# Performance work log

Hardware: AMD Instinct MI355X
Metric: run time of the kernel (lower is better)

Reference implementation:

```python
import jax, jax.numpy as jnp
import numpy as np


def lstm_step(x_t, h, c, Wih, Whh, bih, bhh):
    # PyTorch LSTM gate order: i, f, g, o
    gates = x_t @ Wih.T + h @ Whh.T + bih + bhh
    i, f, g, o = jnp.split(gates, 4, axis=-1)
    i = jax.nn.sigmoid(i)
    f = jax.nn.sigmoid(f)
    g = jnp.tanh(g)
    o = jax.nn.sigmoid(o)
    c_new = f * c + i * g
    h_new = o * jnp.tanh(c_new)
    return h_new, c_new


def setup_inputs() -> dict:
    key = jax.random.key(0)
    N, C, T, V, M = 512, 3, 300, 25, 2
    F = C * V * M  # 150
    H = 100
    ks = jax.random.split(key, 12)
    s = 1.0 / np.sqrt(H)  # PyTorch LSTM/Linear init scale
    u = lambda k, shape: jax.random.uniform(k, shape, jnp.float32, -s, s)
    return {
        "x": jax.random.normal(ks[0], (N, C, T, V, M), jnp.float32),
        "enc_Wih": u(ks[1], (4 * H, F)),
        "enc_Whh": u(ks[2], (4 * H, H)),
        "enc_bih": u(ks[3], (4 * H,)),
        "enc_bhh": u(ks[4], (4 * H,)),
        "dec_Wih": u(ks[5], (4 * H, F)),
        "dec_Whh": u(ks[6], (4 * H, H)),
        "dec_bih": u(ks[7], (4 * H,)),
        "dec_bhh": u(ks[8], (4 * H,)),
        "fc_W": u(ks[9], (F, H)),
        "fc_b": u(ks[10], (F,)),
    }


def reference(x, enc_Wih, enc_Whh, enc_bih, enc_bhh,
              dec_Wih, dec_Whh, dec_bih, dec_bhh, fc_W, fc_b):
    N, C, T, V, M = x.shape
    F = C * V * M
    H = enc_Whh.shape[1]
    # (N,C,T,V,M) -> (N,T,C*V*M)
    xs = jnp.transpose(x, (0, 2, 1, 3, 4)).reshape(N, T, F)

    # Encoder LSTM: only need final (h, c)
    h0 = jnp.zeros((N, H), x.dtype)
    c0 = jnp.zeros((N, H), x.dtype)

    def enc_step(carry, xt):
        h, c = carry
        h, c = lstm_step(xt, h, c, enc_Wih, enc_Whh, enc_bih, enc_bhh)
        return (h, c), None

    (h, c), _ = jax.lax.scan(enc_step, (h0, c0), jnp.swapaxes(xs, 0, 1))

    inp0 = jnp.zeros((N, F), x.dtype)

    def dec_step(carry, _):
        inp, h, c = carry
        h, c = lstm_step(inp, h, c, dec_Wih, dec_Whh, dec_bih, dec_bhh)
        out = h @ fc_W.T + fc_b
        return (out, h, c), out

    _, outs = jax.lax.scan(dec_step, (inp0, h, c), None, length=T - 1)  # [T-1,N,F]

    # outputs[:,0,:] stays zero, like the torch.zeros buffer
    outputs = jnp.concatenate([jnp.zeros((1, N, F), x.dtype), outs], axis=0)  # [T,N,F]
    outputs = jnp.swapaxes(outputs, 0, 1).reshape(N, T, C, V, M)
    return jnp.transpose(outputs, (0, 2, 1, 3, 4))  # (N,C,T,V,M)
```

## Files before the change

### kernel.cpp

```cpp
#include <hip/hip_runtime.h>
#include <hip/hip_fp16.h>


#define B_HIST   0u
#define HIST_STRIDE 29952
#define B_W2S    30670848u
#define B_BEFFS  30830848u
#define B_AWIH   30832448u
#define B_AENC   30975808u
#define B_ADEC1  31090496u
#define B_ADEC2  31205184u
#define B_BENCF  31319872u
#define B_B1F    31348544u
#define B_BEFFF  31377216u
#define B_XG     31405888u
#define XG_PER_BG 4300800u

typedef _Float16 f16x8 __attribute__((ext_vector_type(8)));
typedef float    f32x4 __attribute__((ext_vector_type(4)));

typedef _Float16 h2_t __attribute__((ext_vector_type(2)));
#if defined(__has_builtin)
#if __has_builtin(__builtin_amdgcn_fdot2)
#define HAS_FDOT2 1
#endif
#endif

__device__ __forceinline__ float fdot2u(unsigned a, unsigned b, float c) {
#ifdef HAS_FDOT2
  return __builtin_amdgcn_fdot2(__builtin_bit_cast(h2_t, a), __builtin_bit_cast(h2_t, b), c, false);
#else
  float al = __half2float(__ushort_as_half((unsigned short)(a & 0xffffu)));
  float ah = __half2float(__ushort_as_half((unsigned short)(a >> 16)));
  float bl = __half2float(__ushort_as_half((unsigned short)(b & 0xffffu)));
  float bh = __half2float(__ushort_as_half((unsigned short)(b >> 16)));
  return fmaf(ah, bh, fmaf(al, bl, c));
#endif
}

__device__ __forceinline__ unsigned pkrtz(float a, float b) {
  return __builtin_bit_cast(unsigned, __builtin_amdgcn_cvt_pkrtz(a, b));
}
__device__ __forceinline__ unsigned pack2f(float a, float b) {
  return (unsigned)__half_as_ushort(__float2half(a)) |
         ((unsigned)__half_as_ushort(__float2half(b)) << 16);
}
__device__ __forceinline__ float fast_sig(float x) {
  float e = __builtin_amdgcn_exp2f(x * -1.442695040888963f);
  return __builtin_amdgcn_rcpf(1.f + e);
}
__device__ __forceinline__ float fast_tanh(float x) {
  float e = __builtin_amdgcn_exp2f(x * -2.885390081777926f);
  return fmaf(2.f, __builtin_amdgcn_rcpf(1.f + e), -1.f);
}
__device__ __forceinline__ f32x4 mfma16(uint4 a, uint4 b, f32x4 c) {
  return __builtin_amdgcn_mfma_f32_16x16x32_f16(
      __builtin_bit_cast(f16x8, a), __builtin_bit_cast(f16x8, b), c, 0, 0, 0);
}
__device__ __forceinline__ float uslo(unsigned u) {
  return __half2float(__ushort_as_half((unsigned short)(u & 0xffffu)));
}
__device__ __forceinline__ float ushi(unsigned u) {
  return __half2float(__ushort_as_half((unsigned short)(u >> 16)));
}

__global__ void prep_w2(const float* __restrict__ dWih, const float* __restrict__ dWhh,
                        const float* __restrict__ dbih, const float* __restrict__ dbhh,
                        const float* __restrict__ fcW,  const float* __restrict__ fcb,
                        char* __restrict__ wsb)
{
  int idx = blockIdx.x * 256 + threadIdx.x;
  if (idx < 40000) {
    int r = idx / 100, j = idx - r * 100;
    float s = 0.f;
    for (int f = 0; f < 150; ++f) s = fmaf(dWih[r * 150 + f], fcW[f * 100 + j], s);
    ((float*)(wsb + B_W2S))[idx] = dWhh[r * 100 + j] + s;
  } else if (idx < 40400) {
    int r = idx - 40000;
    float s = 0.f;
    for (int f = 0; f < 150; ++f) s = fmaf(dWih[r * 150 + f], fcb[f], s);
    ((float*)(wsb + B_BEFFS))[r] = dbih[r] + dbhh[r] + s;
  }
}

__global__ void prep_frags(const float* __restrict__ eWih, const float* __restrict__ eWhh,
                           const float* __restrict__ dWhh,
                           const float* __restrict__ ebih, const float* __restrict__ ebhh,
                           const float* __restrict__ dbih, const float* __restrict__ dbhh,
                           char* __restrict__ wsb)
{
  int idx = blockIdx.x * 256 + threadIdx.x;
  const float* w2s = (const float*)(wsb + B_W2S);
  const float* beffs = (const float*)(wsb + B_BEFFS);
  if (idx < 8960) {
    int l = idx & 63, fi = idx >> 6;
    int kc = fi % 5, mt = fi / 5;
    int w = mt >> 2, ty = mt & 3;
    int gr = w * 16 + (l & 15);
    int r = ty * 100 + gr;
    int k0 = kc * 32 + (l >> 4) * 8;
    unsigned u[4];
    for (int p = 0; p < 4; ++p) {
      int k = k0 + 2 * p;
      float v0 = (gr < 100 && k     < 150) ? eWih[r * 150 + k]     : 0.f;
      float v1 = (gr < 100 && k + 1 < 150) ? eWih[r * 150 + k + 1] : 0.f;
      u[p] = pack2f(v0, v1);
    }
    ((uint4*)(wsb + B_AWIH))[idx] = make_uint4(u[0], u[1], u[2], u[3]);
  } else if (idx < 8960 + 3 * 7168) {
    int t = idx - 8960;
    int set = t / 7168, q = t - set * 7168;
    int l = q & 63, fi = q >> 6;
    int kc = fi & 3, mt = fi >> 2;
    int w = mt >> 2, ty = mt & 3;
    int gr = w * 16 + (l & 15);
    int r = ty * 100 + gr;
    int k0 = kc * 32 + (l >> 4) * 8;
    unsigned u[4];
    for (int p = 0; p < 4; ++p) {
      int k = k0 + 2 * p;
      float v0 = 0.f, v1 = 0.f;
      if (gr < 100) {
        if (k < 100)     v0 = set == 0 ? eWhh[r*100+k]   : set == 1 ? dWhh[r*100+k]   : w2s[r*100+k];
        if (k + 1 < 100) v1 = set == 0 ? eWhh[r*100+k+1] : set == 1 ? dWhh[r*100+k+1] : w2s[r*100+k+1];
      }
      u[p] = pack2f(v0, v1);
    }
    ((uint4*)(wsb + B_AENC + (unsigned)set * 114688u))[q] = make_uint4(u[0], u[1], u[2], u[3]);
  } else if (idx < 8960 + 21504 + 3 * 1792) {
    int t = idx - 8960 - 21504;
    int set = t / 1792, q = t - set * 1792;
    int l = q & 63, mt = q >> 6;
    int w = mt >> 2, ty = mt & 3;
    float v[4];
    for (int rr = 0; rr < 4; ++rr) {
      int gr = w * 16 + (l >> 4) * 4 + rr;
      int r = ty * 100 + gr;
      v[rr] = 0.f;
      if (gr < 100)
        v[rr] = set == 0 ? ebih[r] + ebhh[r] : set == 1 ? dbih[r] + dbhh[r] : beffs[r];
    }
    ((float4*)(wsb + B_BENCF + (unsigned)set * 28672u))[q] = make_float4(v[0], v[1], v[2], v[3]);
  }
}

__global__ __launch_bounds__(64)
void pre(const float* __restrict__ x, char* __restrict__ wsb, int nbase)
{
  const int l = threadIdx.x;
  const int tg = blockIdx.x;
  const int b  = blockIdx.y;
  const int quad = l >> 4, nn = l & 15;
  __shared__ unsigned short xls[4][16][168];

  const int t0 = tg * 4;
  const int n0 = nbase + b * 16;
  for (int it = 0; it < 84; ++it) {
    int i = l + it * 64;
    int tp = i / 1344; int rem = i - tp * 1344;
    int np = rem / 84; int p = rem - np * 84;
    unsigned val = 0;
    if (p < 75) {
      int f0 = 2 * p; int c = f0 / 50; int q = f0 - c * 50;
      const float2 v = *(const float2*)(x + (size_t)(n0 + np) * 45000 + c * 15000 + (t0 + tp) * 50 + q);
      val = pkrtz(v.x, v.y);
    }
    *(unsigned*)&xls[tp][np][2 * p] = val;
  }
  __syncthreads();

  uint4 B[4][5];
#pragma unroll
  for (int u = 0; u < 4; ++u)
#pragma unroll
    for (int kc = 0; kc < 5; ++kc)
      B[u][kc] = *(const uint4*)&xls[u][nn][kc * 32 + quad * 8];

  const uint4* awih = (const uint4*)(wsb + B_AWIH);
  const float4* bencf = (const float4*)(wsb + B_BENCF);
  unsigned short* xgo = (unsigned short*)(wsb + B_XG);

  for (int mt = 0; mt < 28; ++mt) {
    const int w = mt >> 2, ty = mt & 3;
    uint4 A0 = awih[(mt * 5 + 0) * 64 + l];
    uint4 A1 = awih[(mt * 5 + 1) * 64 + l];
    uint4 A2 = awih[(mt * 5 + 2) * 64 + l];
    uint4 A3 = awih[(mt * 5 + 3) * 64 + l];
    uint4 A4 = awih[(mt * 5 + 4) * 64 + l];
    float4 bi = bencf[mt * 64 + l];
    f32x4 bias; bias[0] = bi.x; bias[1] = bi.y; bias[2] = bi.z; bias[3] = bi.w;
#pragma unroll
    for (int u = 0; u < 4; ++u) {
      f32x4 acc = bias;
      acc = mfma16(A0, B[u][0], acc);
      acc = mfma16(A1, B[u][1], acc);
      acc = mfma16(A2, B[u][2], acc);
      acc = mfma16(A3, B[u][3], acc);
      acc = mfma16(A4, B[u][4], acc);
      unsigned u0 = pkrtz(acc[0], acc[1]);
      unsigned u1 = pkrtz(acc[2], acc[3]);
      size_t off = ((size_t)(b * 300 + t0 + u) * 7 + w) * 1024 + l * 16 + ty * 4;
      *(uint2*)(xgo + off) = make_uint2(u0, u1);
    }
  }
}

__global__ __launch_bounds__(448)
void recurrent(char* __restrict__ wsb, int nbase)
{
  const int tid = threadIdx.x;
  const int l = tid & 63, w = tid >> 6;
  const int quad = l >> 4, n = l & 15;
  const int c0 = w * 16 + quad * 4;
  __shared__ unsigned short hbuf[2][16][136];

  for (int i = tid; i < 2176; i += 448) ((unsigned*)hbuf)[i] = 0;

  const uint4* aenc  = (const uint4*)(wsb + B_AENC);
  const uint4* adec1 = (const uint4*)(wsb + B_ADEC1);
  const uint4* adec2 = (const uint4*)(wsb + B_ADEC2);
  uint4 A[4][4];
#pragma unroll
  for (int ty = 0; ty < 4; ++ty)
#pragma unroll
    for (int kc = 0; kc < 4; ++kc)
      A[ty][kc] = aenc[((w * 4 + ty) * 4 + kc) * 64 + l];

  f32x4 bias[4];
  float cst[4] = {0.f, 0.f, 0.f, 0.f};

  const uint4* xgw = (const uint4*)(wsb + B_XG) + (size_t)blockIdx.x * 300 * 896 + (w * 64 + l) * 2;
  uint4 xa = xgw[0], xb = xgw[1];

  unsigned short* hist = (unsigned short*)(wsb + B_HIST) +
                         (size_t)(nbase + blockIdx.x * 16 + n) * HIST_STRIDE + c0;
  const bool hist_on = (c0 < 100);

  for (int g = 0; g < 599; ++g) {
    __syncthreads();
    const int rd = g & 1, wr = rd ^ 1;
    uint4 B0 = *(const uint4*)&hbuf[rd][n][0  + quad * 8];
    uint4 B1 = *(const uint4*)&hbuf[rd][n][32 + quad * 8];
    uint4 B2 = *(const uint4*)&hbuf[rd][n][64 + quad * 8];
    uint4 B3 = *(const uint4*)&hbuf[rd][n][96 + quad * 8];

    f32x4 acc[4];
    if (g < 300) {
      acc[0][0] = uslo(xa.x); acc[0][1] = ushi(xa.x); acc[0][2] = uslo(xa.y); acc[0][3] = ushi(xa.y);
      acc[1][0] = uslo(xa.z); acc[1][1] = ushi(xa.z); acc[1][2] = uslo(xa.w); acc[1][3] = ushi(xa.w);
      acc[2][0] = uslo(xb.x); acc[2][1] = ushi(xb.x); acc[2][2] = uslo(xb.y); acc[2][3] = ushi(xb.y);
      acc[3][0] = uslo(xb.z); acc[3][1] = ushi(xb.z); acc[3][2] = uslo(xb.w); acc[3][3] = ushi(xb.w);
      if (g < 299) { const uint4* p = xgw + (size_t)(g + 1) * 896; xa = p[0]; xb = p[1]; }
    } else {
#pragma unroll
      for (int ty = 0; ty < 4; ++ty) acc[ty] = bias[ty];
    }

#pragma unroll
    for (int kc = 0; kc < 4; ++kc) {
      uint4 Bk = (kc == 0) ? B0 : (kc == 1) ? B1 : (kc == 2) ? B2 : B3;
#pragma unroll
      for (int ty = 0; ty < 4; ++ty) acc[ty] = mfma16(A[ty][kc], Bk, acc[ty]);
    }

    float hv[4];
#pragma unroll
    for (int r = 0; r < 4; ++r) {
      float si = fast_sig(acc[0][r]);
      float sf = fast_sig(acc[1][r]);
      float tg = fast_tanh(acc[2][r]);
      float so = fast_sig(acc[3][r]);
      cst[r] = fmaf(sf, cst[r], si * tg);
      hv[r] = so * fast_tanh(cst[r]);
    }
    unsigned u0 = pkrtz(hv[0], hv[1]);
    unsigned u1 = pkrtz(hv[2], hv[3]);
    *(uint2*)&hbuf[wr][n][c0] = make_uint2(u0, u1);
    if (g >= 300 && hist_on)
      *(uint2*)(hist + (size_t)(g - 300) * 100) = make_uint2(u0, u1);

    if (g == 299) {
#pragma unroll
      for (int ty = 0; ty < 4; ++ty) {
#pragma unroll
        for (int kc = 0; kc < 4; ++kc) A[ty][kc] = adec1[((w * 4 + ty) * 4 + kc) * 64 + l];
        float4 bv = ((const float4*)(wsb + B_B1F))[(w * 4 + ty) * 64 + l];
        bias[ty][0] = bv.x; bias[ty][1] = bv.y; bias[ty][2] = bv.z; bias[ty][3] = bv.w;
      }
    } else if (g == 300) {
#pragma unroll
      for (int ty = 0; ty < 4; ++ty) {
#pragma unroll
        for (int kc = 0; kc < 4; ++kc) A[ty][kc] = adec2[((w * 4 + ty) * 4 + kc) * 64 + l];
        float4 bv = ((const float4*)(wsb + B_BEFFF))[(w * 4 + ty) * 64 + l];
        bias[ty][0] = bv.x; bias[ty][1] = bv.y; bias[ty][2] = bv.z; bias[ty][3] = bv.w;
      }
    }
  }
}

__global__ __launch_bounds__(192, 4)
void emit(const char* __restrict__ wsb, const float* __restrict__ fcW,
          const float* __restrict__ fcb, float* __restrict__ out)
{
  const int f = threadIdx.x;
  const int n = blockIdx.x;
  const int z = blockIdx.y;
  __shared__ unsigned short hl[15008];

  const uint4* src = (const uint4*)((const unsigned short*)(wsb + B_HIST) +
                                    (size_t)n * HIST_STRIDE + z * 15000);
  for (int k = f; k < 1875; k += 192) ((uint4*)hl)[k] = src[k];

  const bool on = f < 150;
  unsigned fw[50];
  float biasv = 0.f;
  if (on) {
    const float* fp = fcW + f * 100;
#pragma unroll
    for (int q = 0; q < 50; ++q) fw[q] = pack2f(fp[2 * q], fp[2 * q + 1]);
    biasv = fcb[f];
  }
  __syncthreads();

  if (!on) return;
  const int cc = f / 50, r = f - cc * 50;
  float* ob = out + (size_t)n * 45000 + cc * 15000 + r;
  if (z == 0) ob[0] = 0.f;
  const int rows = z ? 149 : 150;
  for (int tl = 0; tl < rows; ++tl) {
    const uint4* row = (const uint4*)(hl + tl * 100);
    float a0 = biasv, a1 = 0.f, a2 = 0.f, a3 = 0.f;
#pragma unroll
    for (int ch = 0; ch < 12; ++ch) {
      uint4 v = row[ch];
      a0 = fdot2u(fw[4 * ch + 0], v.x, a0);
      a1 = fdot2u(fw[4 * ch + 1], v.y, a1);
      a2 = fdot2u(fw[4 * ch + 2], v.z, a2);
      a3 = fdot2u(fw[4 * ch + 3], v.w, a3);
    }
    uint2 v2 = *(const uint2*)(hl + tl * 100 + 96);
    a0 = fdot2u(fw[48], v2.x, a0);
    a1 = fdot2u(fw[49], v2.y, a1);
    const int tt = z * 150 + tl + 1;
    ob[tt * 50] = (a0 + a1) + (a2 + a3);
  }
}

extern "C" void kernel_launch(void* const* d_in, const int* in_sizes, int n_in,
                              void* d_out, int out_size, void* d_ws, size_t ws_size,
                              hipStream_t stream) {
  const float* x    = (const float*)d_in[0];
  const float* eWih = (const float*)d_in[1];
  const float* eWhh = (const float*)d_in[2];
  const float* ebih = (const float*)d_in[3];
  const float* ebhh = (const float*)d_in[4];
  const float* dWih = (const float*)d_in[5];
  const float* dWhh = (const float*)d_in[6];
  const float* dbih = (const float*)d_in[7];
  const float* dbhh = (const float*)d_in[8];
  const float* fcW  = (const float*)d_in[9];
  const float* fcb  = (const float*)d_in[10];
  float* out = (float*)d_out;
  char* wsb  = (char*)d_ws;

  int npass = 1;
  while (npass < 32) {
    if ((size_t)B_XG + (size_t)(32 / npass) * XG_PER_BG <= ws_size) break;
    npass *= 2;
  }
  const int bg = 32 / npass;

  prep_w2<<<158, 256, 0, stream>>>(dWih, dWhh, dbih, dbhh, fcW, fcb, wsb);
  prep_frags<<<140, 256, 0, stream>>>(eWih, eWhh, dWhh, ebih, ebhh, dbih, dbhh, wsb);
  for (int p = 0; p < npass; ++p) {
    pre<<<dim3(75, bg), 64, 0, stream>>>(x, wsb, p * bg * 16);
    recurrent<<<bg, 448, 0, stream>>>(wsb, p * bg * 16);
  }
  emit<<<dim3(512, 2), 192, 0, stream>>>(wsb, fcW, fcb, out);
}
```

Measured before the change: 1.407 ms.

## Use MFMA for output projection, widen pre stores, deepen xg prefetch

The emit kernel's per-thread fdot2 projection of the hidden history through fc_W is replaced by 16x16x32 fp16 MFMA tiles, with fc_W fragments packed once in prep_frags. The pre kernel now buffers all four gate tiles per wave and writes them as two 16-byte stores instead of several 8-byte stores. The recurrent kernel prefetches input-gate values two steps ahead and swaps __syncthreads for a raw waitcnt+s_barrier. The MFMA emit uses far fewer threads per block (64 versus 192) and scatters its output writes, so the smaller emit cost may be partly offset by those strided stores and lower occupancy.

```diff
diff --git a/kernel.cpp b/kernel.cpp
--- a/kernel.cpp
+++ b/kernel.cpp
@@ -13,30 +13,14 @@
 #define B_BENCF  31319872u
 #define B_B1F    31348544u
 #define B_BEFFF  31377216u
-#define B_XG     31405888u
+#define B_AFCW   31405888u
+#define B_XG     31446848u
 #define XG_PER_BG 4300800u
 
 typedef _Float16 f16x8 __attribute__((ext_vector_type(8)));
 typedef float    f32x4 __attribute__((ext_vector_type(4)));
 
-typedef _Float16 h2_t __attribute__((ext_vector_type(2)));
-#if defined(__has_builtin)
-#if __has_builtin(__builtin_amdgcn_fdot2)
-#define HAS_FDOT2 1
-#endif
-#endif
-
-__device__ __forceinline__ float fdot2u(unsigned a, unsigned b, float c) {
-#ifdef HAS_FDOT2
-  return __builtin_amdgcn_fdot2(__builtin_bit_cast(h2_t, a), __builtin_bit_cast(h2_t, b), c, false);
-#else
-  float al = __half2float(__ushort_as_half((unsigned short)(a & 0xffffu)));
-  float ah = __half2float(__ushort_as_half((unsigned short)(a >> 16)));
-  float bl = __half2float(__ushort_as_half((unsigned short)(b & 0xffffu)));
-  float bh = __half2float(__ushort_as_half((unsigned short)(b >> 16)));
-  return fmaf(ah, bh, fmaf(al, bl, c));
-#endif
-}
+#define WG_BARRIER() asm volatile("s_waitcnt lgkmcnt(0)\n\ts_barrier" ::: "memory")
 
 __device__ __forceinline__ unsigned pkrtz(float a, float b) {
   return __builtin_bit_cast(unsigned, __builtin_amdgcn_cvt_pkrtz(a, b));
@@ -84,7 +68,7 @@
 }
 
 __global__ void prep_frags(const float* __restrict__ eWih, const float* __restrict__ eWhh,
-                           const float* __restrict__ dWhh,
+                           const float* __restrict__ dWhh, const float* __restrict__ fcW,
                            const float* __restrict__ ebih, const float* __restrict__ ebhh,
                            const float* __restrict__ dbih, const float* __restrict__ dbhh,
                            char* __restrict__ wsb)
@@ -141,6 +125,20 @@
         v[rr] = set == 0 ? ebih[r] + ebhh[r] : set == 1 ? dbih[r] + dbhh[r] : beffs[r];
     }
     ((float4*)(wsb + B_BENCF + (unsigned)set * 28672u))[q] = make_float4(v[0], v[1], v[2], v[3]);
+  } else if (idx < 35840 + 2560) {
+    int q2 = idx - 35840;
+    int l = q2 & 63, fi = q2 >> 6;
+    int kc = fi & 3, mt = fi >> 2;
+    int f = mt * 16 + (l & 15);
+    int k0 = kc * 32 + (l >> 4) * 8;
+    unsigned u[4];
+    for (int p = 0; p < 4; ++p) {
+      int k = k0 + 2 * p;
+      float v0 = (f < 150 && k     < 100) ? fcW[f * 100 + k]     : 0.f;
+      float v1 = (f < 150 && k + 1 < 100) ? fcW[f * 100 + k + 1] : 0.f;
+      u[p] = pack2f(v0, v1);
+    }
+    ((uint4*)(wsb + B_AFCW))[q2] = make_uint4(u[0], u[1], u[2], u[3]);
   }
 }
 
@@ -161,7 +159,7 @@
     int np = rem / 84; int p = rem - np * 84;
     unsigned val = 0;
     if (p < 75) {
-      int f0 = 2 * p; int c = f0 / 50; int q = f0 - c * 50;
+      int c = p * 2 / 50; int q = p * 2 - c * 50;
       const float2 v = *(const float2*)(x + (size_t)(n0 + np) * 45000 + c * 15000 + (t0 + tp) * 50 + q);
       val = pkrtz(v.x, v.y);
     }
@@ -180,27 +178,35 @@
   const float4* bencf = (const float4*)(wsb + B_BENCF);
   unsigned short* xgo = (unsigned short*)(wsb + B_XG);
 
-  for (int mt = 0; mt < 28; ++mt) {
-    const int w = mt >> 2, ty = mt & 3;
-    uint4 A0 = awih[(mt * 5 + 0) * 64 + l];
-    uint4 A1 = awih[(mt * 5 + 1) * 64 + l];
-    uint4 A2 = awih[(mt * 5 + 2) * 64 + l];
-    uint4 A3 = awih[(mt * 5 + 3) * 64 + l];
-    uint4 A4 = awih[(mt * 5 + 4) * 64 + l];
-    float4 bi = bencf[mt * 64 + l];
-    f32x4 bias; bias[0] = bi.x; bias[1] = bi.y; bias[2] = bi.z; bias[3] = bi.w;
+  for (int w = 0; w < 7; ++w) {
+    unsigned st[4][8];
+#pragma unroll
+    for (int ty = 0; ty < 4; ++ty) {
+      const int mt = w * 4 + ty;
+      uint4 A0 = awih[(mt * 5 + 0) * 64 + l];
+      uint4 A1 = awih[(mt * 5 + 1) * 64 + l];
+      uint4 A2 = awih[(mt * 5 + 2) * 64 + l];
+      uint4 A3 = awih[(mt * 5 + 3) * 64 + l];
+      uint4 A4 = awih[(mt * 5 + 4) * 64 + l];
+      float4 bi = bencf[mt * 64 + l];
+      f32x4 bias; bias[0] = bi.x; bias[1] = bi.y; bias[2] = bi.z; bias[3] = bi.w;
+#pragma unroll
+      for (int u = 0; u < 4; ++u) {
+        f32x4 acc = bias;
+        acc = mfma16(A0, B[u][0], acc);
+        acc = mfma16(A1, B[u][1], acc);
+        acc = mfma16(A2, B[u][2], acc);
+        acc = mfma16(A3, B[u][3], acc);
+        acc = mfma16(A4, B[u][4], acc);
+        st[u][ty * 2 + 0] = pkrtz(acc[0], acc[1]);
+        st[u][ty * 2 + 1] = pkrtz(acc[2], acc[3]);
+      }
+    }
 #pragma unroll
     for (int u = 0; u < 4; ++u) {
-      f32x4 acc = bias;
-      acc = mfma16(A0, B[u][0], acc);
-      acc = mfma16(A1, B[u][1], acc);
-      acc = mfma16(A2, B[u][2], acc);
-      acc = mfma16(A3, B[u][3], acc);
-      acc = mfma16(A4, B[u][4], acc);
-      unsigned u0 = pkrtz(acc[0], acc[1]);
-      unsigned u1 = pkrtz(acc[2], acc[3]);
-      size_t off = ((size_t)(b * 300 + t0 + u) * 7 + w) * 1024 + l * 16 + ty * 4;
-      *(uint2*)(xgo + off) = make_uint2(u0, u1);
+      size_t off = ((size_t)(b * 300 + t0 + u) * 7 + w) * 1024 + (size_t)l * 16;
+      *(uint4*)(xgo + off)     = make_uint4(st[u][0], st[u][1], st[u][2], st[u][3]);
+      *(uint4*)(xgo + off + 8) = make_uint4(st[u][4], st[u][5], st[u][6], st[u][7]);
     }
   }
 }
@@ -230,14 +236,16 @@
   float cst[4] = {0.f, 0.f, 0.f, 0.f};
 
   const uint4* xgw = (const uint4*)(wsb + B_XG) + (size_t)blockIdx.x * 300 * 896 + (w * 64 + l) * 2;
-  uint4 xa = xgw[0], xb = xgw[1];
+  uint4 pxa[2], pxb[2];
+  pxa[0] = xgw[0];   pxb[0] = xgw[1];
+  pxa[1] = xgw[896]; pxb[1] = xgw[897];
 
   unsigned short* hist = (unsigned short*)(wsb + B_HIST) +
                          (size_t)(nbase + blockIdx.x * 16 + n) * HIST_STRIDE + c0;
   const bool hist_on = (c0 < 100);
 
   for (int g = 0; g < 599; ++g) {
-    __syncthreads();
+    WG_BARRIER();
     const int rd = g & 1, wr = rd ^ 1;
     uint4 B0 = *(const uint4*)&hbuf[rd][n][0  + quad * 8];
     uint4 B1 = *(const uint4*)&hbuf[rd][n][32 + quad * 8];
@@ -246,11 +254,13 @@
 
     f32x4 acc[4];
     if (g < 300) {
+      const int sl = g & 1;
+      uint4 xa = pxa[sl], xb = pxb[sl];
       acc[0][0] = uslo(xa.x); acc[0][1] = ushi(xa.x); acc[0][2] = uslo(xa.y); acc[0][3] = ushi(xa.y);
       acc[1][0] = uslo(xa.z); acc[1][1] = ushi(xa.z); acc[1][2] = uslo(xa.w); acc[1][3] = ushi(xa.w);
       acc[2][0] = uslo(xb.x); acc[2][1] = ushi(xb.x); acc[2][2] = uslo(xb.y); acc[2][3] = ushi(xb.y);
       acc[3][0] = uslo(xb.z); acc[3][1] = ushi(xb.z); acc[3][2] = uslo(xb.w); acc[3][3] = ushi(xb.w);
-      if (g < 299) { const uint4* p = xgw + (size_t)(g + 1) * 896; xa = p[0]; xb = p[1]; }
+      if (g + 2 < 300) { const uint4* p = xgw + (size_t)(g + 2) * 896; pxa[sl] = p[0]; pxb[sl] = p[1]; }
     } else {
 #pragma unroll
       for (int ty = 0; ty < 4; ++ty) acc[ty] = bias[ty];
@@ -299,51 +309,61 @@
   }
 }
 
-__global__ __launch_bounds__(192, 4)
-void emit(const char* __restrict__ wsb, const float* __restrict__ fcW,
-          const float* __restrict__ fcb, float* __restrict__ out)
+__global__ __launch_bounds__(64)
+void emit(const char* __restrict__ wsb, const float* __restrict__ fcb, float* __restrict__ out)
 {
-  const int f = threadIdx.x;
+  const int l = threadIdx.x;
   const int n = blockIdx.x;
-  const int z = blockIdx.y;
-  __shared__ unsigned short hl[15008];
-
-  const uint4* src = (const uint4*)((const unsigned short*)(wsb + B_HIST) +
-                                    (size_t)n * HIST_STRIDE + z * 15000);
-  for (int k = f; k < 1875; k += 192) ((uint4*)hl)[k] = src[k];
-
-  const bool on = f < 150;
-  unsigned fw[50];
-  float biasv = 0.f;
-  if (on) {
-    const float* fp = fcW + f * 100;
-#pragma unroll
-    for (int q = 0; q < 50; ++q) fw[q] = pack2f(fp[2 * q], fp[2 * q + 1]);
-    biasv = fcb[f];
-  }
-  __syncthreads();
-
-  if (!on) return;
-  const int cc = f / 50, r = f - cc * 50;
-  float* ob = out + (size_t)n * 45000 + cc * 15000 + r;
-  if (z == 0) ob[0] = 0.f;
-  const int rows = z ? 149 : 150;
-  for (int tl = 0; tl < rows; ++tl) {
-    const uint4* row = (const uint4*)(hl + tl * 100);
-    float a0 = biasv, a1 = 0.f, a2 = 0.f, a3 = 0.f;
-#pragma unroll
-    for (int ch = 0; ch < 12; ++ch) {
-      uint4 v = row[ch];
-      a0 = fdot2u(fw[4 * ch + 0], v.x, a0);
-      a1 = fdot2u(fw[4 * ch + 1], v.y, a1);
-      a2 = fdot2u(fw[4 * ch + 2], v.z, a2);
-      a3 = fdot2u(fw[4 * ch + 3], v.w, a3);
-    }
-    uint2 v2 = *(const uint2*)(hl + tl * 100 + 96);
-    a0 = fdot2u(fw[48], v2.x, a0);
-    a1 = fdot2u(fw[49], v2.y, a1);
-    const int tt = z * 150 + tl + 1;
-    ob[tt * 50] = (a0 + a1) + (a2 + a3);
+  const int quad = l >> 4, col = l & 15;
+  const uint4* afcw = (const uint4*)(wsb + B_AFCW);
+  const unsigned short* hist_n = (const unsigned short*)(wsb + B_HIST) + (size_t)n * HIST_STRIDE;
+  float* on_ = out + (size_t)n * 45000;
+
+  for (int i = l; i < 150; i += 64) on_[(i / 50) * 15000 + (i % 50)] = 0.f;
+
+  uint4 A[10][4];
+#pragma unroll
+  for (int mt = 0; mt < 10; ++mt)
+#pragma unroll
+    for (int kc = 0; kc < 4; ++kc)
+      A[mt][kc] = afcw[(mt * 4 + kc) * 64 + l];
+
+  float fcbv[10][4];
+#pragma unroll
+  for (int mt = 0; mt < 10; ++mt)
+#pragma unroll
+    for (int r = 0; r < 4; ++r) {
+      int f = mt * 16 + quad * 4 + r;
+      fcbv[mt][r] = (f < 150) ? fcb[f] : 0.f;
+    }
+
+  for (int tt = 0; tt < 19; ++tt) {
+    const int t0 = 1 + tt * 16;
+    const int th = t0 + col - 1;
+    const unsigned short* hb = hist_n + (size_t)th * 100 + quad * 8;
+    uint4 B0 = *(const uint4*)(hb);
+    uint4 B1 = *(const uint4*)(hb + 32);
+    uint4 B2 = *(const uint4*)(hb + 64);
+    uint4 B3 = *(const uint4*)(hb + 96);
+    const int t = t0 + col;
+    const bool ton = (t <= 299);
+#pragma unroll
+    for (int mt = 0; mt < 10; ++mt) {
+      f32x4 acc;
+      acc[0] = fcbv[mt][0]; acc[1] = fcbv[mt][1]; acc[2] = fcbv[mt][2]; acc[3] = fcbv[mt][3];
+      acc = mfma16(A[mt][0], B0, acc);
+      acc = mfma16(A[mt][1], B1, acc);
+      acc = mfma16(A[mt][2], B2, acc);
+      acc = mfma16(A[mt][3], B3, acc);
+#pragma unroll
+      for (int r = 0; r < 4; ++r) {
+        const int f = mt * 16 + quad * 4 + r;
+        if (ton && f < 150) {
+          const int c = f / 50, vm = f - c * 50;
+          on_[c * 15000 + t * 50 + vm] = acc[r];
+        }
+      }
+    }
   }
 }
 
@@ -372,10 +392,10 @@
   const int bg = 32 / npass;
 
   prep_w2<<<158, 256, 0, stream>>>(dWih, dWhh, dbih, dbhh, fcW, fcb, wsb);
-  prep_frags<<<140, 256, 0, stream>>>(eWih, eWhh, dWhh, ebih, ebhh, dbih, dbhh, wsb);
+  prep_frags<<<150, 256, 0, stream>>>(eWih, eWhh, dWhh, fcW, ebih, ebhh, dbih, dbhh, wsb);
   for (int p = 0; p < npass; ++p) {
     pre<<<dim3(75, bg), 64, 0, stream>>>(x, wsb, p * bg * 16);
     recurrent<<<bg, 448, 0, stream>>>(wsb, p * bg * 16);
   }
-  emit<<<dim3(512, 2), 192, 0, stream>>>(wsb, fcW, fcb, out);
-}
+  emit<<<512, 64, 0, stream>>>(wsb, fcb, out);
+}
```

After: 1.189 ms. 1.18x faster.
